# Kernel tuning notes

Hardware: AMD Instinct MI355X
Metric: run time of the kernel (lower is better)

## Reference

```python
import jax, jax.numpy as jnp
import numpy as np

B, C, H, W = 4, 256, 64, 64
HEADS, GROUPS = 8, 8
HEAD_DIM = C // HEADS
EPS_GN = 1e-5
EPS_NORM = 1e-12


def group_norm(x, gamma, beta):
    b, c, h, w = x.shape
    xr = x.reshape(b, GROUPS, c // GROUPS, h, w)
    mean = xr.mean(axis=(2, 3, 4), keepdims=True)
    var = xr.var(axis=(2, 3, 4), keepdims=True)
    xn = ((xr - mean) / jnp.sqrt(var + EPS_GN)).reshape(b, c, h, w)
    return xn * gamma[None, :, None, None] + beta[None, :, None, None]


def conv1x1(x, w):
    # w: (C_out, C_in) pointwise conv
    return jnp.einsum('oc,bchw->bohw', w, x)


def dwconv3x3(x, w, b):
    # depthwise 3x3, w: (C, 1, 3, 3)
    y = jax.lax.conv_general_dilated(
        x, w, window_strides=(1, 1), padding='SAME',
        dimension_numbers=('NCHW', 'OIHW', 'NCHW'),
        feature_group_count=C)
    return y + b[None, :, None, None]


def setup_inputs() -> dict:
    key = jax.random.key(0)
    ks = jax.random.split(key, 7)
    s = 0.05
    f32 = jnp.float32
    return {
        'x': jax.random.normal(ks[0], (B, C, H, W), f32),
        'wq': jax.random.normal(ks[1], (C, C), f32) * s,
        'gq_gamma': jnp.ones((C,), f32), 'gq_beta': jnp.zeros((C,), f32),
        'wk': jax.random.normal(ks[2], (C, C), f32) * s,
        'gk_gamma': jnp.ones((C,), f32), 'gk_beta': jnp.zeros((C,), f32),
        'wv': jax.random.normal(ks[3], (C, C), f32) * s,
        'wp': jax.random.normal(ks[4], (C, C), f32) * s,
        'bp': jnp.zeros((C,), f32),
        'gp_gamma': jnp.ones((C,), f32), 'gp_beta': jnp.zeros((C,), f32),
        'dw1': jax.random.normal(ks[5], (C, 1, 3, 3), f32) * s,
        'db1': jnp.zeros((C,), f32),
        'dw2': jax.random.normal(ks[6], (C, 1, 3, 3), f32) * s,
        'db2': jnp.zeros((C,), f32),
    }


def reference(x, wq, gq_gamma, gq_beta, wk, gk_gamma, gk_beta, wv,
              wp, bp, gp_gamma, gp_beta, dw1, db1, dw2, db2):
    b, c, h, w = x.shape
    q = group_norm(conv1x1(x, wq), gq_gamma, gq_beta)
    k = group_norm(conv1x1(x, wk), gk_gamma, gk_beta)
    v = conv1x1(x, wv)

    def to_tokens(t):
        # (B,C,H,W) -> (B*H*W, heads, head_dim)
        return t.transpose(0, 2, 3, 1).reshape(b * h * w, HEADS, HEAD_DIM)

    q, k, v = to_tokens(q), to_tokens(k), to_tokens(v)
    qn = q / jnp.maximum(jnp.linalg.norm(q, axis=-1, keepdims=True), EPS_NORM)
    kn = k / jnp.maximum(jnp.linalg.norm(k, axis=-1, keepdims=True), EPS_NORM)
    scale = 1.0 / np.sqrt(HEAD_DIM).astype(np.float32)
    # per-pixel spectral attention: (N, heads, d, d)
    attn = jnp.einsum('nhd,nhe->nhde', qn, kn) * scale
    attn = jax.nn.softmax(attn, axis=-1)
    out = jnp.einsum('nhde,nhe->nhd', attn, v)
    out = out.reshape(b, h, w, c).transpose(0, 3, 1, 2)

    pos = dwconv3x3(x, dw1, db1)
    pos = jax.nn.gelu(pos, approximate=False)
    pos = dwconv3x3(pos, dw2, db2)

    out = out + pos
    out = conv1x1(out, wp) + bp[None, :, None, None]
    out = group_norm(out, gp_gamma, gp_beta)
    return out
```

## Files before the change

### kernel.cpp

```cpp
#include <hip/hip_runtime.h>
#include <math.h>
#include <stdint.h>

#define C_ 256
#define HW_ 4096
#define PLANE (C_*HW_)
#define INV_CNT (1.f / 131072.f)
#define NSLOT 16

typedef __attribute__((ext_vector_type(8))) short bf16x8;
typedef __attribute__((ext_vector_type(4))) float f32x4;

__device__ __forceinline__ unsigned short f2bf(float f) {
    union { float f; unsigned int u; } v; v.f = f;
    unsigned int r = v.u + 0x7fffu + ((v.u >> 16) & 1u);
    return (unsigned short)(r >> 16);
}

__device__ __forceinline__ float bf2f(unsigned short u) {
    return __uint_as_float(((unsigned)u) << 16);
}

__device__ __forceinline__ void load_lds16(const void* g, void* l) {
    __builtin_amdgcn_global_load_lds(
        (const __attribute__((address_space(1))) unsigned int*)g,
        (__attribute__((address_space(3))) unsigned int*)l, 16, 0, 0);
}

__global__ __launch_bounds__(256) void transpose_cvt_kernel(
    const float* __restrict__ src, unsigned short* __restrict__ dst,
    const float* __restrict__ wq, const float* __restrict__ wk,
    const float* __restrict__ wv, const float* __restrict__ wp,
    unsigned short* __restrict__ wbf, float* __restrict__ stats)
{
    __shared__ float tile[64][65];
    int t = threadIdx.x;

    int bid = blockIdx.x + 64 * (blockIdx.y + 4 * blockIdx.z);
    {
        int widx = bid * 256 + t;
        const float* s = (widx < 65536) ? wq : (widx < 131072) ? wk
                       : (widx < 196608) ? wv : wp;
        wbf[widx] = f2bf(s[widx & 65535]);
        if (bid == 0) {
#pragma unroll
            for (int i = 0; i < 12; i++) stats[t + i * 256] = 0.f;
        }
    }

    int b = blockIdx.z;
    const float* s = src + (size_t)b * PLANE;
    unsigned short* d = dst + (size_t)b * PLANE;
    int c0 = blockIdx.y * 64, n0 = blockIdx.x * 64;
    int r = t >> 6, col = t & 63;
#pragma unroll
    for (int i = 0; i < 16; i++)
        tile[r + i * 4][col] = s[(size_t)(c0 + r + i * 4) * HW_ + n0 + col];
    __syncthreads();
#pragma unroll
    for (int i = 0; i < 16; i++)
        d[(size_t)(n0 + r + i * 4) * 256 + c0 + col] = f2bf(tile[col][r + i * 4]);
}

__global__ __launch_bounds__(256) void transpose_cvt_add_kernel(
    const unsigned short* __restrict__ pos, const unsigned short* __restrict__ attn,
    unsigned short* __restrict__ dst)
{
    __shared__ float tile[64][65];
    int b = blockIdx.z;
    const unsigned short* s = pos + (size_t)b * PLANE;
    const unsigned short* a = attn + (size_t)b * PLANE;
    unsigned short* d = dst + (size_t)b * PLANE;
    int c0 = blockIdx.y * 64, n0 = blockIdx.x * 64;
    int t = threadIdx.x;
    int r = t >> 6, col = t & 63;
#pragma unroll
    for (int i = 0; i < 16; i++)
        tile[r + i * 4][col] = bf2f(s[(size_t)(c0 + r + i * 4) * HW_ + n0 + col]);
    __syncthreads();
#pragma unroll
    for (int i = 0; i < 16; i++) {
        size_t o = (size_t)(n0 + r + i * 4) * 256 + c0 + col;
        d[o] = f2bf(tile[col][r + i * 4] + bf2f(a[o]));
    }
}

__device__ __forceinline__ void mfma_core(
    const unsigned short* __restrict__ A,
    const unsigned short* __restrict__ Bm,
    int m0, int n0, f32x4 (&acc)[4][4],
    unsigned short* sA, unsigned short* sB)
{
    const int t = threadIdx.x;
    const int lane = t & 63, wave = t >> 6;

#pragma unroll
    for (int i = 0; i < 4; i++)
#pragma unroll
        for (int j = 0; j < 4; j++) acc[i][j] = (f32x4)0.f;

    const int srow = wave * 32 + (lane >> 2);
    const int scol = (lane & 3) * 8;
    const unsigned short* ga = A  + (size_t)(m0 + srow) * 256 + scol;
    const unsigned short* gb = Bm + (size_t)(n0 + srow) * 256 + scol;
    const int lbase = (wave * 32) * 32;

    const int wm = wave >> 1, wn = wave & 1;
    const int fr = lane & 15, kg = lane >> 4;

    for (int k0 = 0; k0 < 256; k0 += 64) {
        if (k0) __syncthreads();
        load_lds16(ga + k0,            sA + lbase);
        load_lds16(ga + k0 + 16 * 256, sA + lbase + 16 * 32);
        load_lds16(gb + k0,            sB + lbase);
        load_lds16(gb + k0 + 16 * 256, sB + lbase + 16 * 32);
        load_lds16(ga + k0 + 32,            sA + 4096 + lbase);
        load_lds16(ga + k0 + 32 + 16 * 256, sA + 4096 + lbase + 16 * 32);
        load_lds16(gb + k0 + 32,            sB + 4096 + lbase);
        load_lds16(gb + k0 + 32 + 16 * 256, sB + 4096 + lbase + 16 * 32);
        __syncthreads();

#pragma unroll
        for (int kk = 0; kk < 2; kk++) {
            bf16x8 af[4], bfr[4];
#pragma unroll
            for (int i = 0; i < 4; i++) {
                af[i]  = *(const bf16x8*)(sA + kk * 4096 + (wm * 64 + i * 16 + fr) * 32 + kg * 8);
                bfr[i] = *(const bf16x8*)(sB + kk * 4096 + (wn * 64 + i * 16 + fr) * 32 + kg * 8);
            }
#pragma unroll
            for (int mi = 0; mi < 4; mi++)
#pragma unroll
                for (int ni = 0; ni < 4; ni++)
                    acc[mi][ni] = __builtin_amdgcn_mfma_f32_16x16x32_bf16(
                        af[mi], bfr[ni], acc[mi][ni], 0, 0, 0);
        }
    }
}

__device__ __forceinline__ void stat_atomic(
    float s0, float ss0, float s1, float ss1, float* d0, float* d1)
{
#pragma unroll
    for (int off = 32; off >= 1; off >>= 1) {
        s0  += __shfl_down(s0, off);  ss0 += __shfl_down(ss0, off);
        s1  += __shfl_down(s1, off);  ss1 += __shfl_down(ss1, off);
    }
    if ((threadIdx.x & 63) == 0) {
        atomicAdd(d0, s0); atomicAdd(d0 + 1, ss0);
        atomicAdd(d1, s1); atomicAdd(d1 + 1, ss1);
    }
}

__device__ __forceinline__ void stat_read(const float* sp, float& S, float& SS) {
    S = 0.f; SS = 0.f;
#pragma unroll
    for (int i = 0; i < NSLOT; i++) { S += sp[i * 2]; SS += sp[i * 2 + 1]; }
}

__device__ __forceinline__ float gelu_exact(float v) {
    return 0.5f * v * (1.f + erff(v * 0.70710678118654752f));
}

__global__ __launch_bounds__(256) void gemm_qkv_dw_kernel(
    const unsigned short* __restrict__ wbf, const unsigned short* __restrict__ xT,
    unsigned short* __restrict__ q, unsigned short* __restrict__ k,
    unsigned short* __restrict__ v, float* __restrict__ stats,
    const float* __restrict__ x,
    const float* __restrict__ dw1, const float* __restrict__ db1,
    const float* __restrict__ dw2, const float* __restrict__ db2,
    unsigned short* __restrict__ pos)
{
    __shared__ __align__(16) char smem[66 * 68 * 4 * 2];
    const int bid = blockIdx.x;
    const int t = threadIdx.x;

    if (bid < 768) {
        unsigned short* sA = (unsigned short*)smem;
        unsigned short* sB = (unsigned short*)(smem + 16384);
        int z = bid >> 6, rr = bid & 63;
        int batch = z & 3, which = z >> 2;
        unsigned short* Y = ((which == 0) ? q : (which == 1) ? k : v)
                            + (size_t)batch * PLANE;
        const unsigned short* A  = wbf + which * 65536;
        const unsigned short* Bm = xT + (size_t)batch * PLANE;
        const int m0 = (rr & 1) * 128;
        const int n0 = (rr >> 1) * 128;

        f32x4 acc[4][4];
        mfma_core(A, Bm, m0, n0, acc, sA, sB);

        const int lane = t & 63, wave = t >> 6;
        const int wm = wave >> 1, wn = wave & 1;
        const int cl = lane & 15, qd = lane >> 4;

        if (which < 2) {
            float s[2] = {0.f, 0.f}, ss[2] = {0.f, 0.f};
#pragma unroll
            for (int mi = 0; mi < 4; mi++)
#pragma unroll
                for (int ni = 0; ni < 4; ni++)
#pragma unroll
                    for (int r = 0; r < 4; r++) {
                        float vv = acc[mi][ni][r];
                        s[mi >> 1] += vv; ss[mi >> 1] += vv * vv;
                    }
            int g0 = (m0 >> 5) + wm * 2;
            int slot = (rr >> 1) & (NSLOT - 1);
            float* d0 = stats + (size_t)(which * 32 + batch * 8 + g0) * (NSLOT * 2) + slot * 2;
            stat_atomic(s[0], ss[0], s[1], ss[1], d0, d0 + NSLOT * 2);
        }

#pragma unroll
        for (int mi = 0; mi < 4; mi++) {
            int oc = m0 + wm * 64 + mi * 16 + qd * 4;
#pragma unroll
            for (int ni = 0; ni < 4; ni++) {
                int token = n0 + wn * 64 + ni * 16 + cl;
                uint2 pk;
                pk.x = (unsigned)f2bf(acc[mi][ni][0]) | ((unsigned)f2bf(acc[mi][ni][1]) << 16);
                pk.y = (unsigned)f2bf(acc[mi][ni][2]) | ((unsigned)f2bf(acc[mi][ni][3]) << 16);
                *(uint2*)&Y[(size_t)token * 256 + oc] = pk;
            }
        }
    } else {
        float* xs = (float*)smem;
        float* ps = xs + 66 * 68;
        const int bc = bid - 768;
        const int c = bc & 255;
        const float* plane = x + (size_t)bc * 4096;

        float w1[9], w2[9];
#pragma unroll
        for (int i = 0; i < 9; i++) { w1[i] = dw1[c * 9 + i]; w2[i] = dw2[c * 9 + i]; }
        const float b1 = db1[c], b2 = db2[c];

        for (int i = t; i < 66 * 66; i += 256) {
            int r = i / 66, cc = i - r * 66;
            int gr = r - 1, gc = cc - 1;
            float vv = 0.f;
            if ((unsigned)gr < 64u && (unsigned)gc < 64u) vv = plane[gr * 64 + gc];
            xs[r * 68 + cc] = vv;
        }
        __syncthreads();

        for (int i = t; i < 66 * 66; i += 256) {
            int pr = i / 66, pc = i - pr * 66;
            int gr = pr - 1, gc = pc - 1;
            float val = 0.f;
            if ((unsigned)gr < 64u && (unsigned)gc < 64u) {
                float s = b1;
#pragma unroll
                for (int ky = 0; ky < 3; ky++)
#pragma unroll
                    for (int kx = 0; kx < 3; kx++)
                        s += w1[ky * 3 + kx] * xs[(gr + ky) * 68 + (gc + kx)];
                val = gelu_exact(s);
            }
            ps[pr * 68 + pc] = val;
        }
        __syncthreads();

        for (int i = t; i < 4096; i += 256) {
            int orow = i >> 6, ocol = i & 63;
            float s = b2;
#pragma unroll
            for (int ky = 0; ky < 3; ky++)
#pragma unroll
                for (int kx = 0; kx < 3; kx++)
                    s += w2[ky * 3 + kx] * ps[(orow + ky) * 68 + (ocol + kx)];
            pos[(size_t)bc * 4096 + i] = f2bf(s);
        }
    }
}

__global__ __launch_bounds__(256) void gemm_out_mfma(
    const unsigned short* __restrict__ wbf, const unsigned short* __restrict__ aT,
    const float* __restrict__ bp, unsigned short* __restrict__ yb,
    float* __restrict__ stats)
{
    __shared__ __align__(16) unsigned short sA[2 * 128 * 32];
    __shared__ __align__(16) unsigned short sB[2 * 128 * 32];
    int batch = blockIdx.z;
    const unsigned short* A  = aT + (size_t)batch * PLANE;
    const unsigned short* Bm = wbf + 3 * 65536;
    unsigned short* Y = yb + (size_t)batch * PLANE;
    const int m0 = blockIdx.x * 128;
    const int n0 = blockIdx.y * 128;

    f32x4 acc[4][4];
    mfma_core(A, Bm, m0, n0, acc, sA, sB);

    const int lane = threadIdx.x & 63, wave = threadIdx.x >> 6;
    const int wm = wave >> 1, wn = wave & 1;
    const int cl = lane & 15, qd = lane >> 4;

    float s[2] = {0.f, 0.f}, ss[2] = {0.f, 0.f};
#pragma unroll
    for (int ni = 0; ni < 4; ni++) {
        int oc = n0 + wn * 64 + ni * 16 + cl;
        float bb = bp[oc];
#pragma unroll
        for (int mi = 0; mi < 4; mi++) {
            int tk = m0 + wm * 64 + mi * 16 + qd * 4;
            float4 o;
            o.x = acc[mi][ni][0] + bb; o.y = acc[mi][ni][1] + bb;
            o.z = acc[mi][ni][2] + bb; o.w = acc[mi][ni][3] + bb;
            s[ni >> 1] += o.x + o.y + o.z + o.w;
            ss[ni >> 1] += o.x * o.x + o.y * o.y + o.z * o.z + o.w * o.w;
            uint2 pk;
            pk.x = (unsigned)f2bf(o.x) | ((unsigned)f2bf(o.y) << 16);
            pk.y = (unsigned)f2bf(o.z) | ((unsigned)f2bf(o.w) << 16);
            *(uint2*)&Y[(size_t)oc * HW_ + tk] = pk;
        }
    }
    int g0 = (n0 >> 5) + wn * 2;
    int slot = blockIdx.x & (NSLOT - 1);
    float* d0 = stats + (size_t)(64 + batch * 8 + g0) * (NSLOT * 2) + slot * 2;
    stat_atomic(s[0], ss[0], s[1], ss[1], d0, d0 + NSLOT * 2);
}

__device__ __forceinline__ void bf16x32_load(const unsigned short* p, float* o) {
    const uint4* u4 = (const uint4*)p;
#pragma unroll
    for (int i = 0; i < 4; i++) {
        uint4 u = u4[i];
        o[i*8+0] = __uint_as_float(u.x << 16); o[i*8+1] = __uint_as_float(u.x & 0xffff0000u);
        o[i*8+2] = __uint_as_float(u.y << 16); o[i*8+3] = __uint_as_float(u.y & 0xffff0000u);
        o[i*8+4] = __uint_as_float(u.z << 16); o[i*8+5] = __uint_as_float(u.z & 0xffff0000u);
        o[i*8+6] = __uint_as_float(u.w << 16); o[i*8+7] = __uint_as_float(u.w & 0xffff0000u);
    }
}

__global__ __launch_bounds__(256) void attn_tok_kernel(
    const unsigned short* __restrict__ qtok, const unsigned short* __restrict__ ktok,
    const unsigned short* __restrict__ vtok, const float* __restrict__ stats,
    const float* __restrict__ gqg, const float* __restrict__ gqb,
    const float* __restrict__ gkg, const float* __restrict__ gkb,
    unsigned short* __restrict__ out)
{
    __shared__ float sqg[256], sqb[256], skg[256], skb[256];
    const int t = threadIdx.x;
    sqg[t] = gqg[t]; sqb[t] = gqb[t]; skg[t] = gkg[t]; skb[t] = gkb[t];
    __syncthreads();

    const int h = t & 7;
    const int pix = blockIdx.x * 32 + (t >> 3);
    const int b = pix >> 12;
    const size_t base = (size_t)pix * 256 + h * 32;
    const float K2 = 0.17677669529663687f * 1.4426950408889634f;

    float a[32], kn[32], vv[32];

    {
        float S, SS;
        stat_read(stats + (size_t)(b * 8 + h) * (NSLOT * 2), S, SS);
        float m = S * INV_CNT;
        float r = rsqrtf(SS * INV_CNT - m * m + 1e-5f);
        float qv[32], ssum = 0.f;
        bf16x32_load(qtok + base, qv);
#pragma unroll
        for (int j = 0; j < 32; j++) {
            float g = r * sqg[h * 32 + j];
            qv[j] = (qv[j] - m) * g + sqb[h * 32 + j];
            ssum = fmaf(qv[j], qv[j], ssum);
        }
        float inv = K2 / fmaxf(sqrtf(ssum), 1e-12f);
#pragma unroll
        for (int j = 0; j < 32; j++) a[j] = qv[j] * inv;
    }
    {
        float S, SS;
        stat_read(stats + (size_t)(32 + b * 8 + h) * (NSLOT * 2), S, SS);
        float m = S * INV_CNT;
        float r = rsqrtf(SS * INV_CNT - m * m + 1e-5f);
        float ssum = 0.f;
        bf16x32_load(ktok + base, kn);
#pragma unroll
        for (int j = 0; j < 32; j++) {
            float g = r * skg[h * 32 + j];
            kn[j] = (kn[j] - m) * g + skb[h * 32 + j];
            ssum = fmaf(kn[j], kn[j], ssum);
        }
        float inv = 1.f / fmaxf(sqrtf(ssum), 1e-12f);
#pragma unroll
        for (int j = 0; j < 32; j++) kn[j] *= inv;
    }
    bf16x32_load(vtok + base, vv);

    uint4* op = (uint4*)(out + base);
#pragma unroll
    for (int di = 0; di < 4; di++) {
        unsigned int od[4];
#pragma unroll
        for (int dp = 0; dp < 4; dp++) {
            float o2[2];
#pragma unroll
            for (int dd = 0; dd < 2; dd++) {
                float ad = a[di * 8 + dp * 2 + dd];
                float num = 0.f, den = 0.f;
#pragma unroll
                for (int e = 0; e < 32; e++) {
                    float w = __builtin_amdgcn_exp2f(ad * kn[e]);
                    num = fmaf(w, vv[e], num);
                    den += w;
                }
                o2[dd] = num / den;
            }
            od[dp] = (unsigned)f2bf(o2[0]) | ((unsigned)f2bf(o2[1]) << 16);
        }
        op[di] = make_uint4(od[0], od[1], od[2], od[3]);
    }
}

__global__ __launch_bounds__(256) void gn_apply_kernel(
    const unsigned short* __restrict__ src, float* __restrict__ y,
    const float* __restrict__ stats,
    const float* __restrict__ gamma, const float* __restrict__ beta)
{
    int i4 = blockIdx.x * 256 + threadIdx.x;
    int idx = i4 * 4;
    int c = (idx >> 12) & 255;
    int bg = ((idx >> 20) << 3) | (c >> 5);
    float S, SS;
    stat_read(stats + (size_t)(64 + bg) * (NSLOT * 2), S, SS);
    float mean = S * INV_CNT;
    float rstd = rsqrtf(SS * INV_CNT - mean * mean + 1e-5f);
    float ga = rstd * gamma[c], be = beta[c] - mean * ga;
    uint2 u = *(const uint2*)&src[idx];
    float4 v4;
    v4.x = bf2f((unsigned short)(u.x & 0xffff)) * ga + be;
    v4.y = bf2f((unsigned short)(u.x >> 16))    * ga + be;
    v4.z = bf2f((unsigned short)(u.y & 0xffff)) * ga + be;
    v4.w = bf2f((unsigned short)(u.y >> 16))    * ga + be;
    *(float4*)&y[idx] = v4;
}

extern "C" void kernel_launch(void* const* d_in, const int* in_sizes, int n_in,
                              void* d_out, int out_size, void* d_ws, size_t ws_size,
                              hipStream_t stream)
{
    const float* x   = (const float*)d_in[0];
    const float* wq  = (const float*)d_in[1];
    const float* gqg = (const float*)d_in[2];
    const float* gqb = (const float*)d_in[3];
    const float* wk  = (const float*)d_in[4];
    const float* gkg = (const float*)d_in[5];
    const float* gkb = (const float*)d_in[6];
    const float* wv  = (const float*)d_in[7];
    const float* wp  = (const float*)d_in[8];
    const float* bp  = (const float*)d_in[9];
    const float* gpg = (const float*)d_in[10];
    const float* gpb = (const float*)d_in[11];
    const float* dw1 = (const float*)d_in[12];
    const float* db1 = (const float*)d_in[13];
    const float* dw2 = (const float*)d_in[14];
    const float* db2 = (const float*)d_in[15];
    float* out = (float*)d_out;

    char* ws = (char*)d_ws;
    const size_t MB8 = (size_t)8 * 1024 * 1024;
    unsigned short* qtok = (unsigned short*)(ws);
    unsigned short* ktok = (unsigned short*)(ws + MB8);
    unsigned short* vtok = (unsigned short*)(ws + 2 * MB8);
    unsigned short* atok = (unsigned short*)(ws + 3 * MB8);
    unsigned short* xT   = (unsigned short*)(ws + 4 * MB8);
    unsigned short* aT   = xT;
    unsigned short* outb = ktok;
    unsigned short* wbf  = (unsigned short*)(ws + 5 * MB8);
    float*          stats= (float*)(ws + 5 * MB8 + 524288);
    unsigned short* pos  = (unsigned short*)(ws + 6 * MB8);

    dim3 blk(256);
    transpose_cvt_kernel<<<dim3(64, 4, 4), blk, 0, stream>>>(x, xT, wq, wk, wv, wp, wbf, stats);
    gemm_qkv_dw_kernel<<<dim3(1792), blk, 0, stream>>>(wbf, xT, qtok, ktok, vtok, stats,
                                                       x, dw1, db1, dw2, db2, pos);
    attn_tok_kernel<<<dim3(512), blk, 0, stream>>>(qtok, ktok, vtok, stats,
                                                   gqg, gqb, gkg, gkb, atok);
    transpose_cvt_add_kernel<<<dim3(64, 4, 4), blk, 0, stream>>>(pos, atok, aT);
    gemm_out_mfma<<<dim3(32, 2, 4), blk, 0, stream>>>(wbf, aT, bp, outb, stats);
    gn_apply_kernel<<<dim3(4096), blk, 0, stream>>>(outb, out, stats, gpg, gpb);
}
```

Measured before the change: 182.0 us.

## Fuse positional add into attention kernel and split dwconv from QKV GEMM

Drops the separate transpose+add kernel. The attention kernel now loads a channel-major tile of the positional-conv output, transposes it through LDS, and adds it before writing token-major output straight into the out-projection input buffer. The depthwise conv chain moves out of the combined GEMM launch into its own kernel, and the QKV GEMM becomes a standalone kernel with a 3D grid and a smaller LDS footprint. This removes a full read/write pass over the attention output and one launch, at the cost of an extra launch and lost overlap between the GEMM and the conv work that used to share one grid.

```diff
diff --git a/kernel.cpp b/kernel.cpp
--- a/kernel.cpp
+++ b/kernel.cpp
@@ -7,6 +7,7 @@
 #define PLANE (C_*HW_)
 #define INV_CNT (1.f / 131072.f)
 #define NSLOT 16
+#define PSTRIDE 264
 
 typedef __attribute__((ext_vector_type(8))) short bf16x8;
 typedef __attribute__((ext_vector_type(4))) float f32x4;
@@ -60,29 +61,6 @@
 #pragma unroll
     for (int i = 0; i < 16; i++)
         d[(size_t)(n0 + r + i * 4) * 256 + c0 + col] = f2bf(tile[col][r + i * 4]);
-}
-
-__global__ __launch_bounds__(256) void transpose_cvt_add_kernel(
-    const unsigned short* __restrict__ pos, const unsigned short* __restrict__ attn,
-    unsigned short* __restrict__ dst)
-{
-    __shared__ float tile[64][65];
-    int b = blockIdx.z;
-    const unsigned short* s = pos + (size_t)b * PLANE;
-    const unsigned short* a = attn + (size_t)b * PLANE;
-    unsigned short* d = dst + (size_t)b * PLANE;
-    int c0 = blockIdx.y * 64, n0 = blockIdx.x * 64;
-    int t = threadIdx.x;
-    int r = t >> 6, col = t & 63;
-#pragma unroll
-    for (int i = 0; i < 16; i++)
-        tile[r + i * 4][col] = bf2f(s[(size_t)(c0 + r + i * 4) * HW_ + n0 + col]);
-    __syncthreads();
-#pragma unroll
-    for (int i = 0; i < 16; i++) {
-        size_t o = (size_t)(n0 + r + i * 4) * 256 + c0 + col;
-        d[o] = f2bf(tile[col][r + i * 4] + bf2f(a[o]));
-    }
 }
 
 __device__ __forceinline__ void mfma_core(
@@ -158,118 +136,56 @@
     for (int i = 0; i < NSLOT; i++) { S += sp[i * 2]; SS += sp[i * 2 + 1]; }
 }
 
-__device__ __forceinline__ float gelu_exact(float v) {
-    return 0.5f * v * (1.f + erff(v * 0.70710678118654752f));
-}
-
-__global__ __launch_bounds__(256) void gemm_qkv_dw_kernel(
+__global__ __launch_bounds__(256) void gemm_qkv_mfma(
     const unsigned short* __restrict__ wbf, const unsigned short* __restrict__ xT,
     unsigned short* __restrict__ q, unsigned short* __restrict__ k,
-    unsigned short* __restrict__ v, float* __restrict__ stats,
-    const float* __restrict__ x,
-    const float* __restrict__ dw1, const float* __restrict__ db1,
-    const float* __restrict__ dw2, const float* __restrict__ db2,
-    unsigned short* __restrict__ pos)
-{
-    __shared__ __align__(16) char smem[66 * 68 * 4 * 2];
-    const int bid = blockIdx.x;
-    const int t = threadIdx.x;
-
-    if (bid < 768) {
-        unsigned short* sA = (unsigned short*)smem;
-        unsigned short* sB = (unsigned short*)(smem + 16384);
-        int z = bid >> 6, rr = bid & 63;
-        int batch = z & 3, which = z >> 2;
-        unsigned short* Y = ((which == 0) ? q : (which == 1) ? k : v)
-                            + (size_t)batch * PLANE;
-        const unsigned short* A  = wbf + which * 65536;
-        const unsigned short* Bm = xT + (size_t)batch * PLANE;
-        const int m0 = (rr & 1) * 128;
-        const int n0 = (rr >> 1) * 128;
-
-        f32x4 acc[4][4];
-        mfma_core(A, Bm, m0, n0, acc, sA, sB);
-
-        const int lane = t & 63, wave = t >> 6;
-        const int wm = wave >> 1, wn = wave & 1;
-        const int cl = lane & 15, qd = lane >> 4;
-
-        if (which < 2) {
-            float s[2] = {0.f, 0.f}, ss[2] = {0.f, 0.f};
-#pragma unroll
-            for (int mi = 0; mi < 4; mi++)
-#pragma unroll
-                for (int ni = 0; ni < 4; ni++)
-#pragma unroll
-                    for (int r = 0; r < 4; r++) {
-                        float vv = acc[mi][ni][r];
-                        s[mi >> 1] += vv; ss[mi >> 1] += vv * vv;
-                    }
-            int g0 = (m0 >> 5) + wm * 2;
-            int slot = (rr >> 1) & (NSLOT - 1);
-            float* d0 = stats + (size_t)(which * 32 + batch * 8 + g0) * (NSLOT * 2) + slot * 2;
-            stat_atomic(s[0], ss[0], s[1], ss[1], d0, d0 + NSLOT * 2);
-        }
-
-#pragma unroll
-        for (int mi = 0; mi < 4; mi++) {
-            int oc = m0 + wm * 64 + mi * 16 + qd * 4;
-#pragma unroll
-            for (int ni = 0; ni < 4; ni++) {
-                int token = n0 + wn * 64 + ni * 16 + cl;
-                uint2 pk;
-                pk.x = (unsigned)f2bf(acc[mi][ni][0]) | ((unsigned)f2bf(acc[mi][ni][1]) << 16);
-                pk.y = (unsigned)f2bf(acc[mi][ni][2]) | ((unsigned)f2bf(acc[mi][ni][3]) << 16);
-                *(uint2*)&Y[(size_t)token * 256 + oc] = pk;
-            }
-        }
-    } else {
-        float* xs = (float*)smem;
-        float* ps = xs + 66 * 68;
-        const int bc = bid - 768;
-        const int c = bc & 255;
-        const float* plane = x + (size_t)bc * 4096;
-
-        float w1[9], w2[9];
-#pragma unroll
-        for (int i = 0; i < 9; i++) { w1[i] = dw1[c * 9 + i]; w2[i] = dw2[c * 9 + i]; }
-        const float b1 = db1[c], b2 = db2[c];
-
-        for (int i = t; i < 66 * 66; i += 256) {
-            int r = i / 66, cc = i - r * 66;
-            int gr = r - 1, gc = cc - 1;
-            float vv = 0.f;
-            if ((unsigned)gr < 64u && (unsigned)gc < 64u) vv = plane[gr * 64 + gc];
-            xs[r * 68 + cc] = vv;
-        }
-        __syncthreads();
-
-        for (int i = t; i < 66 * 66; i += 256) {
-            int pr = i / 66, pc = i - pr * 66;
-            int gr = pr - 1, gc = pc - 1;
-            float val = 0.f;
-            if ((unsigned)gr < 64u && (unsigned)gc < 64u) {
-                float s = b1;
-#pragma unroll
-                for (int ky = 0; ky < 3; ky++)
-#pragma unroll
-                    for (int kx = 0; kx < 3; kx++)
-                        s += w1[ky * 3 + kx] * xs[(gr + ky) * 68 + (gc + kx)];
-                val = gelu_exact(s);
-            }
-            ps[pr * 68 + pc] = val;
-        }
-        __syncthreads();
-
-        for (int i = t; i < 4096; i += 256) {
-            int orow = i >> 6, ocol = i & 63;
-            float s = b2;
-#pragma unroll
-            for (int ky = 0; ky < 3; ky++)
-#pragma unroll
-                for (int kx = 0; kx < 3; kx++)
-                    s += w2[ky * 3 + kx] * ps[(orow + ky) * 68 + (ocol + kx)];
-            pos[(size_t)bc * 4096 + i] = f2bf(s);
+    unsigned short* __restrict__ v, float* __restrict__ stats)
+{
+    __shared__ __align__(16) unsigned short sA[2 * 128 * 32];
+    __shared__ __align__(16) unsigned short sB[2 * 128 * 32];
+    int z = blockIdx.z;
+    int batch = z & 3, which = z >> 2;
+    unsigned short* Y = ((which == 0) ? q : (which == 1) ? k : v)
+                        + (size_t)batch * PLANE;
+    const unsigned short* A  = wbf + which * 65536;
+    const unsigned short* Bm = xT + (size_t)batch * PLANE;
+    const int m0 = blockIdx.x * 128;
+    const int n0 = blockIdx.y * 128;
+
+    f32x4 acc[4][4];
+    mfma_core(A, Bm, m0, n0, acc, sA, sB);
+
+    const int lane = threadIdx.x & 63, wave = threadIdx.x >> 6;
+    const int wm = wave >> 1, wn = wave & 1;
+    const int cl = lane & 15, qd = lane >> 4;
+
+    if (which < 2) {
+        float s[2] = {0.f, 0.f}, ss[2] = {0.f, 0.f};
+#pragma unroll
+        for (int mi = 0; mi < 4; mi++)
+#pragma unroll
+            for (int ni = 0; ni < 4; ni++)
+#pragma unroll
+                for (int r = 0; r < 4; r++) {
+                    float vv = acc[mi][ni][r];
+                    s[mi >> 1] += vv; ss[mi >> 1] += vv * vv;
+                }
+        int g0 = (m0 >> 5) + wm * 2;
+        int slot = blockIdx.y & (NSLOT - 1);
+        float* d0 = stats + (size_t)(which * 32 + batch * 8 + g0) * (NSLOT * 2) + slot * 2;
+        stat_atomic(s[0], ss[0], s[1], ss[1], d0, d0 + NSLOT * 2);
+    }
+
+#pragma unroll
+    for (int mi = 0; mi < 4; mi++) {
+        int oc = m0 + wm * 64 + mi * 16 + qd * 4;
+#pragma unroll
+        for (int ni = 0; ni < 4; ni++) {
+            int token = n0 + wn * 64 + ni * 16 + cl;
+            uint2 pk;
+            pk.x = (unsigned)f2bf(acc[mi][ni][0]) | ((unsigned)f2bf(acc[mi][ni][1]) << 16);
+            pk.y = (unsigned)f2bf(acc[mi][ni][2]) | ((unsigned)f2bf(acc[mi][ni][3]) << 16);
+            *(uint2*)&Y[(size_t)token * 256 + oc] = pk;
         }
     }
 }
@@ -334,23 +250,47 @@
 
 __global__ __launch_bounds__(256) void attn_tok_kernel(
     const unsigned short* __restrict__ qtok, const unsigned short* __restrict__ ktok,
-    const unsigned short* __restrict__ vtok, const float* __restrict__ stats,
+    const unsigned short* __restrict__ vtok, const unsigned short* __restrict__ pos,
+    const float* __restrict__ stats,
     const float* __restrict__ gqg, const float* __restrict__ gqb,
     const float* __restrict__ gkg, const float* __restrict__ gkb,
     unsigned short* __restrict__ out)
 {
     __shared__ float sqg[256], sqb[256], skg[256], skb[256];
+    __shared__ unsigned short ptile[32 * PSTRIDE];
     const int t = threadIdx.x;
     sqg[t] = gqg[t]; sqb[t] = gqb[t]; skg[t] = gkg[t]; skb[t] = gkb[t];
+
+    const int pix0 = blockIdx.x * 32;
+    const int b = pix0 >> 12;
+    const int n0 = pix0 & 4095;
+
+    {
+        const uint4* prow = (const uint4*)(pos + (size_t)b * PLANE + (size_t)t * HW_ + n0);
+#pragma unroll
+        for (int i = 0; i < 4; i++) {
+            uint4 u = prow[i];
+            ptile[(i*8+0) * PSTRIDE + t] = (unsigned short)(u.x & 0xffff);
+            ptile[(i*8+1) * PSTRIDE + t] = (unsigned short)(u.x >> 16);
+            ptile[(i*8+2) * PSTRIDE + t] = (unsigned short)(u.y & 0xffff);
+            ptile[(i*8+3) * PSTRIDE + t] = (unsigned short)(u.y >> 16);
+            ptile[(i*8+4) * PSTRIDE + t] = (unsigned short)(u.z & 0xffff);
+            ptile[(i*8+5) * PSTRIDE + t] = (unsigned short)(u.z >> 16);
+            ptile[(i*8+6) * PSTRIDE + t] = (unsigned short)(u.w & 0xffff);
+            ptile[(i*8+7) * PSTRIDE + t] = (unsigned short)(u.w >> 16);
+        }
+    }
     __syncthreads();
 
     const int h = t & 7;
-    const int pix = blockIdx.x * 32 + (t >> 3);
-    const int b = pix >> 12;
+    const int p = t >> 3;
+    const int pix = pix0 + p;
     const size_t base = (size_t)pix * 256 + h * 32;
     const float K2 = 0.17677669529663687f * 1.4426950408889634f;
 
-    float a[32], kn[32], vv[32];
+    float a[32], kn[32], vv[32], pv[32];
+
+    bf16x32_load((const unsigned short*)&ptile[p * PSTRIDE + h * 32], pv);
 
     {
         float S, SS;
@@ -397,7 +337,8 @@
             float o2[2];
 #pragma unroll
             for (int dd = 0; dd < 2; dd++) {
-                float ad = a[di * 8 + dp * 2 + dd];
+                int d = di * 8 + dp * 2 + dd;
+                float ad = a[d];
                 float num = 0.f, den = 0.f;
 #pragma unroll
                 for (int e = 0; e < 32; e++) {
@@ -405,11 +346,71 @@
                     num = fmaf(w, vv[e], num);
                     den += w;
                 }
-                o2[dd] = num / den;
+                o2[dd] = num / den + pv[d];
             }
             od[dp] = (unsigned)f2bf(o2[0]) | ((unsigned)f2bf(o2[1]) << 16);
         }
         op[di] = make_uint4(od[0], od[1], od[2], od[3]);
+    }
+}
+
+__device__ __forceinline__ float gelu_exact(float v) {
+    return 0.5f * v * (1.f + erff(v * 0.70710678118654752f));
+}
+
+__global__ __launch_bounds__(256) void dwconv_fused_kernel(
+    const float* __restrict__ x,
+    const float* __restrict__ dw1, const float* __restrict__ db1,
+    const float* __restrict__ dw2, const float* __restrict__ db2,
+    unsigned short* __restrict__ pos)
+{
+    __shared__ float xs[66 * 68];
+    __shared__ float ps[66 * 68];
+    const int bc = blockIdx.x;
+    const int c = bc & 255;
+    const int t = threadIdx.x;
+    const float* plane = x + (size_t)bc * 4096;
+
+    float w1[9], w2[9];
+#pragma unroll
+    for (int i = 0; i < 9; i++) { w1[i] = dw1[c * 9 + i]; w2[i] = dw2[c * 9 + i]; }
+    const float b1 = db1[c], b2 = db2[c];
+
+    for (int i = t; i < 66 * 66; i += 256) {
+        int r = i / 66, cc = i - r * 66;
+        int gr = r - 1, gc = cc - 1;
+        float v = 0.f;
+        if ((unsigned)gr < 64u && (unsigned)gc < 64u) v = plane[gr * 64 + gc];
+        xs[r * 68 + cc] = v;
+    }
+    __syncthreads();
+
+    for (int i = t; i < 66 * 66; i += 256) {
+        int pr = i / 66, pc = i - pr * 66;
+        int gr = pr - 1, gc = pc - 1;
+        float val = 0.f;
+        if ((unsigned)gr < 64u && (unsigned)gc < 64u) {
+            float s = b1;
+#pragma unroll
+            for (int ky = 0; ky < 3; ky++)
+#pragma unroll
+                for (int kx = 0; kx < 3; kx++)
+                    s += w1[ky * 3 + kx] * xs[(gr + ky) * 68 + (gc + kx)];
+            val = gelu_exact(s);
+        }
+        ps[pr * 68 + pc] = val;
+    }
+    __syncthreads();
+
+    for (int i = t; i < 4096; i += 256) {
+        int orow = i >> 6, ocol = i & 63;
+        float s = b2;
+#pragma unroll
+        for (int ky = 0; ky < 3; ky++)
+#pragma unroll
+            for (int kx = 0; kx < 3; kx++)
+                s += w2[ky * 3 + kx] * ps[(orow + ky) * 68 + (ocol + kx)];
+        pos[(size_t)bc * 4096 + i] = f2bf(s);
     }
 }
 
@@ -463,21 +464,19 @@
     unsigned short* qtok = (unsigned short*)(ws);
     unsigned short* ktok = (unsigned short*)(ws + MB8);
     unsigned short* vtok = (unsigned short*)(ws + 2 * MB8);
-    unsigned short* atok = (unsigned short*)(ws + 3 * MB8);
-    unsigned short* xT   = (unsigned short*)(ws + 4 * MB8);
+    unsigned short* xT   = (unsigned short*)(ws + 3 * MB8);
     unsigned short* aT   = xT;
     unsigned short* outb = ktok;
+    unsigned short* pos  = (unsigned short*)(ws + 4 * MB8);
     unsigned short* wbf  = (unsigned short*)(ws + 5 * MB8);
     float*          stats= (float*)(ws + 5 * MB8 + 524288);
-    unsigned short* pos  = (unsigned short*)(ws + 6 * MB8);
 
     dim3 blk(256);
     transpose_cvt_kernel<<<dim3(64, 4, 4), blk, 0, stream>>>(x, xT, wq, wk, wv, wp, wbf, stats);
-    gemm_qkv_dw_kernel<<<dim3(1792), blk, 0, stream>>>(wbf, xT, qtok, ktok, vtok, stats,
-                                                       x, dw1, db1, dw2, db2, pos);
-    attn_tok_kernel<<<dim3(512), blk, 0, stream>>>(qtok, ktok, vtok, stats,
-                                                   gqg, gqb, gkg, gkb, atok);
-    transpose_cvt_add_kernel<<<dim3(64, 4, 4), blk, 0, stream>>>(pos, atok, aT);
+    dwconv_fused_kernel<<<dim3(1024), blk, 0, stream>>>(x, dw1, db1, dw2, db2, pos);
+    gemm_qkv_mfma<<<dim3(2, 32, 12), blk, 0, stream>>>(wbf, xT, qtok, ktok, vtok, stats);
+    attn_tok_kernel<<<dim3(512), blk, 0, stream>>>(qtok, ktok, vtok, pos, stats,
+                                                   gqg, gqb, gkg, gkb, aT);
     gemm_out_mfma<<<dim3(32, 2, 4), blk, 0, stream>>>(wbf, aT, bp, outb, stats);
     gn_apply_kernel<<<dim3(4096), blk, 0, stream>>>(outb, out, stats, gpg, gpb);
 }
```

Measured after the change: 173.3 us. 4.8% less time.
